# Optimization experiments

Measured on AMD Instinct MI355X. Metric: run time of the kernel, lower is better.

The kernel has to match this reference:

```python
import jax, jax.numpy as jnp
import numpy as np

_T_DURATION = 0.2
_C = 0.206756


def setup_inputs() -> dict:
    key = jax.random.key(0)
    k1, k2, k3, k4 = jax.random.split(key, 4)
    B, Nt = 512, 32768
    # normalised params (unused by the analytic path, kept for signature fidelity)
    h = jax.random.normal(k1, (B, 3), dtype=jnp.float32)
    # uniform time grid over the PFWD pulse duration [0, 0.2] s
    t = jnp.linspace(0.0, _T_DURATION, Nt, dtype=jnp.float32)
    # pressure history ~ typical PFWD peak 150 kPa, non-negative half-sine-ish pulse
    u = jax.random.uniform(k2, (B, Nt), dtype=jnp.float32)
    pulse = jnp.sin(jnp.pi * t / _T_DURATION)[None, :]  # (1, Nt) in [0,1]
    p = 150000.0 * pulse * (0.8 + 0.4 * u)  # Pa, peak ~150 kPa
    # physical params inside documented ranges: E1 [1e8,2e9], E2 [1e7,2e8], eta [1e4,5e6]
    r = jax.random.uniform(k3, (B, 3), dtype=jnp.float32)
    lo = jnp.array([1.0e8, 1.0e7, 1.0e4], dtype=jnp.float32)
    hi = jnp.array([2.0e9, 2.0e8, 5.0e6], dtype=jnp.float32)
    h_raw = lo + r * (hi - lo)
    return {"h": h, "t": t, "p": p, "h_raw": h_raw}


def reference(h, t, p, h_raw):
    """omega_i = sum_{j<=i} g(t_i - t_j) * dp_j,
    g(tau) = C*[1/(E1+E2) + E1/(E2*(E1+E2))*(1 - exp(-alpha*tau))],
    alpha  = E1*E2 / ((E1+E2)*eta).
    Exact O(Nt) reformulation: g = (A+D) - D*exp(-alpha*tau) with
    A = C/(E1+E2), D = C*E1/(E2*(E1+E2)), so
    omega_i = (A+D)*p_i - D*s_i,  s_i = exp(-alpha*dt_i)*s_{i-1} + dp_i.
    """
    E1, E2, eta = h_raw[:, 0], h_raw[:, 1], h_raw[:, 2]  # (B,)
    alpha = E1 * E2 / ((E1 + E2) * eta)                   # (B,)
    A = _C / (E1 + E2)                                    # (B,)
    D = _C * E1 / (E2 * (E1 + E2))                        # (B,)
    dp = jnp.diff(p, axis=1, prepend=0.0)                 # (B, Nt), dp_0 = p_0
    dt = jnp.diff(t, prepend=t[0])                        # (Nt,),  dt_0 = 0
    decay = jnp.exp(-alpha[:, None] * dt[None, :])        # (B, Nt)

    def step(s, xs):
        d, dpi = xs                                       # each (B,)
        s = d * s + dpi
        return s, s

    s0 = jnp.zeros(p.shape[0], dtype=p.dtype)
    _, s = jax.lax.scan(step, s0, (decay.T, dp.T))        # s: (Nt, B)
    s = s.T                                               # (B, Nt)
    omega = (A + D)[:, None] * p - D[:, None] * s         # (B, Nt), metres
    return omega
```

## Files before the change

### kernel.cpp

```cpp
#include <hip/hip_runtime.h>

#define TPB 512
#define ROUNDS 16
#define RELEMS (TPB * 4)
#define WAVE 64
#define NW (TPB / WAVE)

__global__ __launch_bounds__(TPB, 4)
void fused_scan(const float* __restrict__ tt, const float* __restrict__ p,
                const float* __restrict__ h_raw, float* __restrict__ out, int Nt)
{
    const int row  = blockIdx.x;
    const int t    = threadIdx.x;
    const int lane = t & (WAVE - 1);
    const int wid  = t >> 6;

    const float E1  = h_raw[row * 3 + 0];
    const float E2  = h_raw[row * 3 + 1];
    const float eta = h_raw[row * 3 + 2];
    const float alpha = (E1 * E2) / ((E1 + E2) * eta);
    const float A = 0.206756f / (E1 + E2);
    const float D = 0.206756f * E1 / (E2 * (E1 + E2));
    const float dtm = (tt[Nt - 1] - tt[0]) / (float)(Nt - 1);
    const float omd = -expm1f(-alpha * dtm);
    const float d   = 1.0f - omd;
    const float K1  = (A + D) - D / d;
    const float K2  = D * omd / d;

    const float d4 = (d * d) * (d * d);
    float d256 = d4;
    #pragma unroll
    for (int i = 0; i < 6; ++i) d256 *= d256;
    float d4l = 1.0f;
    {
        float b = d4;
        #pragma unroll
        for (int i = 0; i < 6; ++i) { if (lane & (1 << i)) d4l *= b; b *= b; }
    }
    float d256w = 1.0f;
    {
        float b = d256;
        #pragma unroll
        for (int i = 0; i < 3; ++i) { if (wid & (1 << i)) d256w *= b; b *= b; }
    }

    const long long base = (long long)row * (long long)Nt;
    const float4* pg = reinterpret_cast<const float4*>(p + base);
    float4*       og = reinterpret_cast<float4*>(out + base);

    float4 v[ROUNDS];
    #pragma unroll
    for (int r = 0; r < ROUNDS; ++r) v[r] = pg[r * TPB + t];

    __shared__ float sw[2][NW];
    __shared__ float cb[2];
    if (t == 0) cb[0] = 0.0f;

    #pragma unroll
    for (int r = 0; r < ROUNDS; ++r) {
        const float4 pv = v[r];

        const float T = fmaf(fmaf(fmaf(pv.x, d, pv.y), d, pv.z), d, pv.w);

        float x = T, m = d4;
        #pragma unroll
        for (int k = 1; k < WAVE; k <<= 1) {
            const float y = __shfl_up(x, k);
            if (lane >= k) x = fmaf(m, y, x);
            m *= m;
        }
        float wave_excl = __shfl_up(x, 1);
        if (lane == 0) wave_excl = 0.0f;
        if (lane == WAVE - 1) sw[r & 1][wid] = x;
        __syncthreads();

        float E = 0.0f;
        for (int w = 0; w < wid; ++w) E = fmaf(d256, E, sw[r & 1][w]);
        const float c    = cb[r & 1];
        const float seed = fmaf(fmaf(c, d256w, E), d4l, wave_excl);

        float W = seed;
        float4 o;
        W = fmaf(W, d, pv.x); o.x = fmaf(K2, W, K1 * pv.x);
        W = fmaf(W, d, pv.y); o.y = fmaf(K2, W, K1 * pv.y);
        W = fmaf(W, d, pv.z); o.z = fmaf(K2, W, K1 * pv.z);
        W = fmaf(W, d, pv.w); o.w = fmaf(K2, W, K1 * pv.w);
        og[r * TPB + t] = o;

        if (t == TPB - 1) cb[(r + 1) & 1] = W;
    }
}

extern "C" void kernel_launch(void* const* d_in, const int* in_sizes, int n_in,
                              void* d_out, int out_size, void* d_ws, size_t ws_size,
                              hipStream_t stream)
{
    const float* tt    = (const float*)d_in[1];
    const float* p     = (const float*)d_in[2];
    const float* h_raw = (const float*)d_in[3];
    float* out = (float*)d_out;

    const int Nt = in_sizes[1];
    const int B  = in_sizes[2] / Nt;
    if (Nt != ROUNDS * RELEMS) return;

    fused_scan<<<B, TPB, 0, stream>>>(tt, p, h_raw, out, Nt);
}
```

Baseline: 29.19 us.

## Batch all rounds' wave scans and use a single barrier with register carry

```diff
diff --git a/kernel.cpp b/kernel.cpp
--- a/kernel.cpp
+++ b/kernel.cpp
@@ -2,7 +2,6 @@
 
 #define TPB 512
 #define ROUNDS 16
-#define RELEMS (TPB * 4)
 #define WAVE 64
 #define NW (TPB / WAVE)
 
@@ -28,20 +27,11 @@
     const float K2  = D * omd / d;
 
     const float d4 = (d * d) * (d * d);
-    float d256 = d4;
-    #pragma unroll
-    for (int i = 0; i < 6; ++i) d256 *= d256;
     float d4l = 1.0f;
     {
         float b = d4;
         #pragma unroll
         for (int i = 0; i < 6; ++i) { if (lane & (1 << i)) d4l *= b; b *= b; }
-    }
-    float d256w = 1.0f;
-    {
-        float b = d256;
-        #pragma unroll
-        for (int i = 0; i < 3; ++i) { if (wid & (1 << i)) d256w *= b; b *= b; }
     }
 
     const long long base = (long long)row * (long long)Nt;
@@ -52,33 +42,56 @@
     #pragma unroll
     for (int r = 0; r < ROUNDS; ++r) v[r] = pg[r * TPB + t];
 
-    __shared__ float sw[2][NW];
-    __shared__ float cb[2];
-    if (t == 0) cb[0] = 0.0f;
+    float x[ROUNDS];
+    #pragma unroll
+    for (int r = 0; r < ROUNDS; ++r)
+        x[r] = fmaf(fmaf(fmaf(v[r].x, d, v[r].y), d, v[r].z), d, v[r].w);
 
+    float m = d4;
+    #pragma unroll
+    for (int k = 1; k < WAVE; k <<= 1) {
+        #pragma unroll
+        for (int r = 0; r < ROUNDS; ++r) {
+            const float y = __shfl_up(x[r], k);
+            if (lane >= k) x[r] = fmaf(m, y, x[r]);
+        }
+        m *= m;
+    }
+    const float d256 = m;
+    float d256w = 1.0f;
+    {
+        float b = d256;
+        #pragma unroll
+        for (int i = 0; i < 3; ++i) { if (wid & (1 << i)) d256w *= b; b *= b; }
+    }
+    float d2048 = d256;
+    d2048 *= d2048; d2048 *= d2048; d2048 *= d2048;
+
+    __shared__ float sw[ROUNDS][NW];
+    if (lane == WAVE - 1) {
+        #pragma unroll
+        for (int r = 0; r < ROUNDS; ++r) sw[r][wid] = x[r];
+    }
+    __syncthreads();
+
+    float C = 0.0f;
     #pragma unroll
     for (int r = 0; r < ROUNDS; ++r) {
+        const float4 sA = *reinterpret_cast<const float4*>(&sw[r][0]);
+        const float4 sB = *reinterpret_cast<const float4*>(&sw[r][4]);
+        float run = 0.0f, E = 0.0f;
+        #define STEP(w, val) { if (wid == (w)) E = run; run = fmaf(d256, run, (val)); }
+        STEP(0, sA.x) STEP(1, sA.y) STEP(2, sA.z) STEP(3, sA.w)
+        STEP(4, sB.x) STEP(5, sB.y) STEP(6, sB.z) STEP(7, sB.w)
+        #undef STEP
+        const float Bt = run;
+
+        float wexcl = __shfl_up(x[r], 1);
+        if (lane == 0) wexcl = 0.0f;
+
+        const float seed = fmaf(fmaf(C, d256w, E), d4l, wexcl);
+
         const float4 pv = v[r];
-
-        const float T = fmaf(fmaf(fmaf(pv.x, d, pv.y), d, pv.z), d, pv.w);
-
-        float x = T, m = d4;
-        #pragma unroll
-        for (int k = 1; k < WAVE; k <<= 1) {
-            const float y = __shfl_up(x, k);
-            if (lane >= k) x = fmaf(m, y, x);
-            m *= m;
-        }
-        float wave_excl = __shfl_up(x, 1);
-        if (lane == 0) wave_excl = 0.0f;
-        if (lane == WAVE - 1) sw[r & 1][wid] = x;
-        __syncthreads();
-
-        float E = 0.0f;
-        for (int w = 0; w < wid; ++w) E = fmaf(d256, E, sw[r & 1][w]);
-        const float c    = cb[r & 1];
-        const float seed = fmaf(fmaf(c, d256w, E), d4l, wave_excl);
-
         float W = seed;
         float4 o;
         W = fmaf(W, d, pv.x); o.x = fmaf(K2, W, K1 * pv.x);
@@ -87,7 +100,7 @@
         W = fmaf(W, d, pv.w); o.w = fmaf(K2, W, K1 * pv.w);
         og[r * TPB + t] = o;
 
-        if (t == TPB - 1) cb[(r + 1) & 1] = W;
+        C = fmaf(d2048, C, Bt);
     }
 }
 
@@ -102,7 +115,7 @@
 
     const int Nt = in_sizes[1];
     const int B  = in_sizes[2] / Nt;
-    if (Nt != ROUNDS * RELEMS) return;
+    if (Nt != ROUNDS * TPB * 4) return;
 
     fused_scan<<<B, TPB, 0, stream>>>(tt, p, h_raw, out, Nt);
 }
```

New measurement: 24.75 us. -15.2%, faster.

## Replace per-round block barriers with a shared-memory two-level scan

Applied to the files above, without the earlier changes.

```diff
diff --git a/kernel.cpp b/kernel.cpp
--- a/kernel.cpp
+++ b/kernel.cpp
@@ -2,9 +2,10 @@
 
 #define TPB 512
 #define ROUNDS 16
-#define RELEMS (TPB * 4)
 #define WAVE 64
 #define NW (TPB / WAVE)
+
+__device__ __forceinline__ int swz(int s) { return s ^ ((s >> 3) & 7); }
 
 __global__ __launch_bounds__(TPB, 4)
 void fused_scan(const float* __restrict__ tt, const float* __restrict__ p,
@@ -27,21 +28,19 @@
     const float K1  = (A + D) - D / d;
     const float K2  = D * omd / d;
 
-    const float d4 = (d * d) * (d * d);
-    float d256 = d4;
+    const float d4  = (d * d) * (d * d);
+    const float d8  = d4 * d4;
+    const float d16 = d8 * d8;
+    const float d32 = d16 * d16;
+    const float inv_d32 = 1.0f / d32;
+    float d2048 = d32;
     #pragma unroll
-    for (int i = 0; i < 6; ++i) d256 *= d256;
-    float d4l = 1.0f;
+    for (int i = 0; i < 6; ++i) d2048 *= d2048;
+    float d4t = 1.0f;
     {
         float b = d4;
         #pragma unroll
-        for (int i = 0; i < 6; ++i) { if (lane & (1 << i)) d4l *= b; b *= b; }
-    }
-    float d256w = 1.0f;
-    {
-        float b = d256;
-        #pragma unroll
-        for (int i = 0; i < 3; ++i) { if (wid & (1 << i)) d256w *= b; b *= b; }
+        for (int i = 0; i < 9; ++i) { if (t & (1 << i)) d4t *= b; b *= b; }
     }
 
     const long long base = (long long)row * (long long)Nt;
@@ -52,33 +51,66 @@
     #pragma unroll
     for (int r = 0; r < ROUNDS; ++r) v[r] = pg[r * TPB + t];
 
-    __shared__ float sw[2][NW];
-    __shared__ float cb[2];
-    if (t == 0) cb[0] = 0.0f;
+    __shared__ float sBuf[ROUNDS * TPB];
+    __shared__ float sBt[ROUNDS];
+
+    const int myAddr4 = swz(t >> 2) * 4 + (t & 3);
+    #pragma unroll
+    for (int r = 0; r < ROUNDS; ++r) {
+        const float T = fmaf(fmaf(fmaf(v[r].x, d, v[r].y), d, v[r].z), d, v[r].w);
+        sBuf[r * TPB + myAddr4] = T;
+    }
+    __syncthreads();
 
     #pragma unroll
-    for (int r = 0; r < ROUNDS; ++r) {
-        const float4 pv = v[r];
-
-        const float T = fmaf(fmaf(fmaf(pv.x, d, pv.y), d, pv.z), d, pv.w);
-
-        float x = T, m = d4;
+    for (int j = 0; j < 2; ++j) {
+        const int r = 2 * wid + j;
+        const float4 ta = *reinterpret_cast<const float4*>(&sBuf[r * TPB + swz(2 * lane)     * 4]);
+        const float4 tb = *reinterpret_cast<const float4*>(&sBuf[r * TPB + swz(2 * lane + 1) * 4]);
+        float L = ta.x;
+        L = fmaf(L, d4, ta.y); L = fmaf(L, d4, ta.z); L = fmaf(L, d4, ta.w);
+        L = fmaf(L, d4, tb.x); L = fmaf(L, d4, tb.y); L = fmaf(L, d4, tb.z);
+        L = fmaf(L, d4, tb.w);
+        float x = L, m = d32;
         #pragma unroll
         for (int k = 1; k < WAVE; k <<= 1) {
             const float y = __shfl_up(x, k);
             if (lane >= k) x = fmaf(m, y, x);
             m *= m;
         }
-        float wave_excl = __shfl_up(x, 1);
-        if (lane == 0) wave_excl = 0.0f;
-        if (lane == WAVE - 1) sw[r & 1][wid] = x;
-        __syncthreads();
+        const float prev = (x - L) * inv_d32;
+        float4 oa, ob;
+        float s = prev;
+        oa.x = s; s = fmaf(s, d4, ta.x);
+        oa.y = s; s = fmaf(s, d4, ta.y);
+        oa.z = s; s = fmaf(s, d4, ta.z);
+        oa.w = s; s = fmaf(s, d4, ta.w);
+        ob.x = s; s = fmaf(s, d4, tb.x);
+        ob.y = s; s = fmaf(s, d4, tb.y);
+        ob.z = s; s = fmaf(s, d4, tb.z);
+        ob.w = s;
+        *reinterpret_cast<float4*>(&sBuf[r * TPB + swz(2 * lane)     * 4]) = oa;
+        *reinterpret_cast<float4*>(&sBuf[r * TPB + swz(2 * lane + 1) * 4]) = ob;
+        if (lane == WAVE - 1) sBt[r] = x;
+    }
+    __syncthreads();
 
-        float E = 0.0f;
-        for (int w = 0; w < wid; ++w) E = fmaf(d256, E, sw[r & 1][w]);
-        const float c    = cb[r & 1];
-        const float seed = fmaf(fmaf(c, d256w, E), d4l, wave_excl);
-
+    float Bt[ROUNDS];
+    {
+        const float4 b0 = *reinterpret_cast<const float4*>(&sBt[0]);
+        const float4 b1 = *reinterpret_cast<const float4*>(&sBt[4]);
+        const float4 b2 = *reinterpret_cast<const float4*>(&sBt[8]);
+        const float4 b3 = *reinterpret_cast<const float4*>(&sBt[12]);
+        Bt[0]=b0.x; Bt[1]=b0.y; Bt[2]=b0.z;  Bt[3]=b0.w;
+        Bt[4]=b1.x; Bt[5]=b1.y; Bt[6]=b1.z;  Bt[7]=b1.w;
+        Bt[8]=b2.x; Bt[9]=b2.y; Bt[10]=b2.z; Bt[11]=b2.w;
+        Bt[12]=b3.x;Bt[13]=b3.y;Bt[14]=b3.z; Bt[15]=b3.w;
+    }
+    float C = 0.0f;
+    #pragma unroll
+    for (int r = 0; r < ROUNDS; ++r) {
+        const float seed = fmaf(C, d4t, sBuf[r * TPB + myAddr4]);
+        const float4 pv = v[r];
         float W = seed;
         float4 o;
         W = fmaf(W, d, pv.x); o.x = fmaf(K2, W, K1 * pv.x);
@@ -86,8 +118,7 @@
         W = fmaf(W, d, pv.z); o.z = fmaf(K2, W, K1 * pv.z);
         W = fmaf(W, d, pv.w); o.w = fmaf(K2, W, K1 * pv.w);
         og[r * TPB + t] = o;
-
-        if (t == TPB - 1) cb[(r + 1) & 1] = W;
+        C = fmaf(d2048, C, Bt[r]);
     }
 }
 
@@ -102,7 +133,7 @@
 
     const int Nt = in_sizes[1];
     const int B  = in_sizes[2] / Nt;
-    if (Nt != ROUNDS * RELEMS) return;
+    if (Nt != ROUNDS * TPB * 4) return;
 
     fused_scan<<<B, TPB, 0, stream>>>(tt, p, h_raw, out, Nt);
 }
```

Measured after the change: 25.44 us. 12.8% less time.
